# Performance work log

Hardware: AMD Instinct MI355X
Metric: run time of the kernel (lower is better)

Reference implementation:

```python
import jax, jax.numpy as jnp
import numpy as np

B, N, DIM = 1, 1024, 2048
HEADS, KV_HEADS, DH = 16, 2, 128
GQ = HEADS // KV_HEADS
CMP_BLK, CMP_STRIDE = 32, 16
SEL_BLK, N_SEL = 64, 4
WIN = 128
MEM_KV = 1
SCALE = DH ** -0.5
NEG = -1e10


def rmsnorm(x, g):
    return x * jax.lax.rsqrt(jnp.mean(x * x, axis=-1, keepdims=True) + 1e-6) * g


def rope(x):
    # interleaved rotary (rotary-embedding-torch convention), theta=10000
    n, d = x.shape[-2], x.shape[-1]
    inv = 1.0 / (10000.0 ** (jnp.arange(0, d, 2, dtype=jnp.float32) / d))
    ang = jnp.arange(n, dtype=jnp.float32)[:, None] * inv  # (n, d/2)
    cos, sin = jnp.cos(ang), jnp.sin(ang)
    x1, x2 = x[..., 0::2], x[..., 1::2]
    return jnp.stack([x1 * cos - x2 * sin, x1 * sin + x2 * cos], axis=-1).reshape(x.shape)


def _gqa_attend(q, k, v):
    # q: (B, HEADS, N, DH); k, v: (B, KV_HEADS, J, DH). heads split h-major into (kv_h, gq).
    qg = q.reshape(B, KV_HEADS, GQ, N, DH)
    sim = jnp.einsum('bhgnd,bhjd->bhgnj', qg, k) * SCALE
    attn = jax.nn.softmax(sim, axis=-1)
    out = jnp.einsum('bhgnj,bhjd->bhgnd', attn, v)
    return out.reshape(B, HEADS, N, DH), sim


def _fwd(x, g_norm, W_qkv, k_pos, v_pos, mem_kv, Wk1, bk1, Wk2, bk2, Wv1, bv1, Wv2, bv2, Wg, bg, W_out):
    dim_inner = HEADS * DH
    dim_kv = KV_HEADS * DH
    xn = rmsnorm(x, g_norm)
    qkv = xn @ W_qkv
    q, k, v = jnp.split(qkv, [dim_inner, dim_inner + dim_kv], axis=-1)
    q = q.reshape(B, N, HEADS, DH).transpose(0, 2, 1, 3)
    k = k.reshape(B, N, KV_HEADS, DH).transpose(0, 2, 1, 3)
    v = v.reshape(B, N, KV_HEADS, DH).transpose(0, 2, 1, 3)

    # ---- compressed branch (pre-rotary q/k): overlapping windows -> MLP per block ----
    ov = CMP_BLK - CMP_STRIDE
    n_win = N // CMP_STRIDE
    widx = jnp.arange(n_win)[:, None] * CMP_STRIDE + jnp.arange(CMP_BLK)[None, :]
    kp = jnp.pad(k, ((0, 0), (0, 0), (ov, 0), (0, 0)))
    vp = jnp.pad(v, ((0, 0), (0, 0), (ov, 0), (0, 0)))
    kwin = kp[:, :, widx, :] + k_pos[None, :, None]  # (B,KV,n_win,CMP_BLK,DH)
    vwin = vp[:, :, widx, :] + v_pos[None, :, None]

    def mlp(w, W1, b1, W2, b2):
        f = w.reshape(B, KV_HEADS, n_win, CMP_BLK * DH)
        return jax.nn.relu(f @ W1 + b1) @ W2 + b2

    ck = mlp(kwin, Wk1, bk1, Wk2, bk2)
    cv = mlp(vwin, Wv1, bv1, Wv2, bv2)
    ck = jnp.concatenate([jnp.broadcast_to(mem_kv[0][None], (B, KV_HEADS, MEM_KV, DH)), ck], axis=2)
    cv = jnp.concatenate([jnp.broadcast_to(mem_kv[1][None], (B, KV_HEADS, MEM_KV, DH)), cv], axis=2)
    cmp_out, csim = _gqa_attend(q, ck, cv)

    # ---- rotary embeddings for fine + sliding branches ----
    q = rope(q)
    k = rope(k)

    # ---- top-k block selection from compressed similarities ----
    n_fine = N // SEL_BLK
    cpf = SEL_BLK // CMP_STRIDE
    imp = csim[..., MEM_KV:].mean(axis=2)  # (B,KV,N,n_win): mean over grouped queries
    imp = imp.reshape(B, KV_HEADS, N, n_fine, cpf).mean(axis=-1)
    qi = jnp.arange(N) // SEL_BLK
    diag = qi[:, None] == jnp.arange(n_fine)[None, :]
    imp = jnp.where(diag, NEG, imp)  # own block masked out of scoring
    imp = jax.nn.softmax(jnp.pad(imp, ((0, 0), (0, 0), (0, 0), (1, 0)), constant_values=-1000.0), axis=-1)[..., 1:]
    _, sel = jax.lax.top_k(imp, N_SEL)  # (B,KV,N,N_SEL)
    own = jnp.broadcast_to(qi[None, None, :, None], (B, KV_HEADS, N, 1))
    sel = jnp.concatenate([sel, own], axis=-1)  # always attend the query's own block

    # ---- fine (selected-block) attention ----
    kb = k.reshape(B, KV_HEADS, n_fine, SEL_BLK, DH)
    vb = v.reshape(B, KV_HEADS, n_fine, SEL_BLK, DH)
    gather = jax.vmap(jax.vmap(lambda blocks, idx: blocks[idx]))  # over B, KV_HEADS
    t_tot = (N_SEL + 1) * SEL_BLK
    fk = gather(kb, sel).reshape(B, KV_HEADS, N, t_tot, DH)
    fv = gather(vb, sel).reshape(B, KV_HEADS, N, t_tot, DH)
    qg = q.reshape(B, KV_HEADS, GQ, N, DH)
    fsim = jnp.einsum('bhgnd,bhntd->bhgnt', qg, fk) * SCALE
    fattn = jax.nn.softmax(fsim, axis=-1)
    fine_out = jnp.einsum('bhgnt,bhntd->bhgnd', fattn, fv).reshape(B, HEADS, N, DH)

    # ---- sliding window attention (non-causal, exact windowsize) ----
    kf = jnp.repeat(k, GQ, axis=1)
    vf = jnp.repeat(v, GQ, axis=1)
    nb = N // WIN
    qb = q.reshape(B, HEADS, nb, WIN, DH)
    kpad = jnp.pad(kf, ((0, 0), (0, 0), (WIN, WIN), (0, 0))).reshape(B, HEADS, nb + 2, WIN, DH)
    vpad = jnp.pad(vf, ((0, 0), (0, 0), (WIN, WIN), (0, 0))).reshape(B, HEADS, nb + 2, WIN, DH)
    kwin3 = jnp.concatenate([kpad[:, :, i:i + nb] for i in range(3)], axis=3)  # (B,H,nb,3W,DH)
    vwin3 = jnp.concatenate([vpad[:, :, i:i + nb] for i in range(3)], axis=3)
    qoff = jnp.arange(WIN)
    koff = jnp.arange(3 * WIN) - WIN
    rel_ok = jnp.abs(qoff[:, None] - koff[None, :]) <= WIN  # (W, 3W)
    kglob = jnp.arange(nb)[:, None] * WIN + koff[None, :]
    in_range = (kglob >= 0) & (kglob < N)  # (nb, 3W)
    mask = rel_ok[None, :, :] & in_range[:, None, :]  # (nb, W, 3W)
    ssim = jnp.einsum('bhnid,bhnjd->bhnij', qb, kwin3) * SCALE
    ssim = jnp.where(mask, ssim, NEG)
    sattn = jax.nn.softmax(ssim, axis=-1)
    slide_out = jnp.einsum('bhnij,bhnjd->bhnid', sattn, vwin3).reshape(B, HEADS, N, DH)

    # ---- learned sigmoid gate combine: (compressed, fine, sliding) ----
    gates = jax.nn.sigmoid(xn @ Wg + bg).reshape(B, N, HEADS, 3).transpose(0, 2, 1, 3)
    out = cmp_out * gates[..., 0:1] + fine_out * gates[..., 1:2] + slide_out * gates[..., 2:3]
    out = out.transpose(0, 2, 1, 3).reshape(B, N, HEADS * DH)
    return out @ W_out


def setup_inputs():
    key = jax.random.key(0)
    ks = jax.random.split(key, 12)
    s = 0.02
    dim_inner, dim_kv, cdim = HEADS * DH, KV_HEADS * DH, CMP_BLK * DH
    rn = lambda k, shape: jax.random.normal(k, shape, jnp.float32) * s
    return {
        'x': jax.random.normal(ks[0], (B, N, DIM), jnp.float32),
        'g_norm': jnp.ones((DIM,), jnp.float32),
        'W_qkv': rn(ks[1], (DIM, dim_inner + 2 * dim_kv)),
        'k_pos': rn(ks[2], (KV_HEADS, CMP_BLK, DH)),
        'v_pos': rn(ks[3], (KV_HEADS, CMP_BLK, DH)),
        'mem_kv': rn(ks[4], (2, KV_HEADS, MEM_KV, DH)),
        'Wk1': rn(ks[5], (cdim, cdim)), 'bk1': jnp.zeros((cdim,), jnp.float32),
        'Wk2': rn(ks[6], (cdim, DH)), 'bk2': jnp.zeros((DH,), jnp.float32),
        'Wv1': rn(ks[7], (cdim, cdim)), 'bv1': jnp.zeros((cdim,), jnp.float32),
        'Wv2': rn(ks[8], (cdim, DH)), 'bv2': jnp.zeros((DH,), jnp.float32),
        'Wg': rn(ks[9], (DIM, 3 * HEADS)),
        'bg': jnp.tile(jnp.array([-2.0, -2.0, 2.0], jnp.float32), HEADS),
        'W_out': rn(ks[10], (dim_inner, DIM)),
    }


def reference(x, g_norm, W_qkv, k_pos, v_pos, mem_kv, Wk1, bk1, Wk2, bk2, Wv1, bv1, Wv2, bv2, Wg, bg, W_out):
    return _fwd(x, g_norm, W_qkv, k_pos, v_pos, mem_kv, Wk1, bk1, Wk2, bk2, Wv1, bv1, Wv2, bv2, Wg, bg, W_out)
```

## Files before the change

### kernel.cpp

```cpp
#include <hip/hip_runtime.h>
#include <hip/hip_bf16.h>
#include <math.h>

typedef __hip_bfloat16 bf16;
typedef __attribute__((ext_vector_type(8))) short bf16x8;
typedef __attribute__((ext_vector_type(4))) float f32x4;

#define N_TOK 1024
#define DIM 2048
#define NHEADS 16
#define KVH 2
#define DH 128
#define GQ 8
#define NWIN 64
#define CMP_BLK 32
#define NCMP 65
#define NFINE 16
#define SEL_BLK 64
#define T_TOT 320
#define CDIM 4096
#define SCALE 0.08838834764831845f

static __device__ __forceinline__ float b2f(bf16 v){ return __bfloat162float(v); }
static __device__ __forceinline__ float bfbits2f(unsigned int u){
// ... 130 lines not shown
  float* C           = kvsel ? cvb : ckb;
  __shared__ __align__(16) float As[16*68];
  __shared__ __align__(16) float Bs[16*68];
  int tid = threadIdx.x;
  int tx = tid & 15, ty = tid >> 4;
  int m0 = blockIdx.y * 64, n0 = blockIdx.x * 64;
  float c[4][4] = {};
  for (int k0 = kz; k0 < kz + 128; k0 += 16){
    #pragma unroll
    for (int i = 0; i < 4; ++i){
      int idx = tid + i*256;
      int kk = idx & 15, m = idx >> 4;
      float av = Af[(size_t)(m0+m)*CDIM + k0 + kk];
      av = fmaxf(av + afold[k0+kk], 0.f);
      As[kk*68 + m] = av;
    }
    #pragma unroll
    for (int i = 0; i < 4; ++i){
      int idx = tid + i*256;
      int nn = idx & 63, kk = idx >> 6;
      Bs[kk*68 + nn] = B[(size_t)(k0+kk)*DH + n0 + nn];
    }
    __syncthreads();
    #pragma unroll
    for (int kk = 0; kk < 16; ++kk){
      float a[4], b[4];
      *(float4*)a = *(const float4*)&As[kk*68 + ty*4];
      *(float4*)b = *(const float4*)&Bs[kk*68 + tx*4];
      #pragma unroll
      for (int i = 0; i < 4; ++i)
        #pragma unroll
        for (int j = 0; j < 4; ++j)
          c[i][j] += a[i]*b[j];
    }
    __syncthreads();
  }
  #pragma unroll
  for (int i = 0; i < 4; ++i){
    int row = m0 + ty*4 + i;
    #pragma unroll
    for (int j = 0; j < 4; ++j){
      int col = n0 + tx*4 + j;
      atomicAdd(&C[(size_t)row*DH + col], c[i][j]);
    }
  }
}

__global__ __launch_bounds__(256) void gemm_mfma_mlp1_kernel(const unsigned short* __restrict__ fh,
                                                             const unsigned short* __restrict__ fl,
                                                             const float* __restrict__ Wk1,
                                                             const float* __restrict__ Wv1,
                                                             float* __restrict__ hbuf2){
  const int kvsel = blockIdx.z >> 3;
  const int kz = (blockIdx.z & 7) * 512;
  const unsigned short* Ah = fh + (size_t)kvsel*128*CDIM;
  const unsigned short* Al = fl + (size_t)kvsel*128*CDIM;
  const float* B = kvsel ? Wv1 : Wk1;
  float* C = hbuf2 + (size_t)kvsel*128*CDIM;
  const int n0 = blockIdx.x * 64;
  const int m0 = blockIdx.y * 32;
  const int tid = threadIdx.x;
  const int wid = tid >> 6, lane = tid & 63;
  const int l15 = lane & 15, lg = lane >> 4;
  const int colL = wid*16 + l15;
  __shared__ __align__(16) float Bs[2][32][68];

  f32x4 acc[2];
  #pragma unroll
  for (int m = 0; m < 2; ++m) acc[m] = (f32x4){0.f,0.f,0.f,0.f};

  const unsigned short* ahp[2];
  const unsigned short* alp[2];
  #pragma unroll
  for (int m = 0; m < 2; ++m){
    size_t ro = (size_t)(m0 + m*16 + l15)*CDIM + kz + lg*8;
    ahp[m] = Ah + ro;
    alp[m] = Al + ro;
  }
  const int sr = tid >> 3, sc = (tid & 7) * 8;

  float4 rb0, rb1;
  int4 rah[2], ral[2];
  {
    const float* bp = B + (size_t)(kz + sr)*CDIM + n0 + sc;
    rb0 = *(const float4*)(bp);
    rb1 = *(const float4*)(bp + 4);
    #pragma unroll
    for (int m = 0; m < 2; ++m){
      rah[m] = *(const int4*)(ahp[m]);
      ral[m] = *(const int4*)(alp[m]);
    }
  }

  #pragma unroll 1
  for (int s = 0; s < 16; ++s){
    const int buf = s & 1;
    *(float4*)&Bs[buf][sr][sc]     = rb0;
    *(float4*)&Bs[buf][sr][sc + 4] = rb1;
    int4 cah[2], cal[2];
    #pragma unroll
    for (int m = 0; m < 2; ++m){ cah[m] = rah[m]; cal[m] = ral[m]; }
    __syncthreads();
    if (s + 1 < 16){
      const int kr = kz + (s+1)*32;
      const float* bp = B + (size_t)(kr + sr)*CDIM + n0 + sc;
      rb0 = *(const float4*)(bp);
      rb1 = *(const float4*)(bp + 4);
      #pragma unroll
      for (int m = 0; m < 2; ++m){
        rah[m] = *(const int4*)(ahp[m] + (s+1)*32);
        ral[m] = *(const int4*)(alp[m] + (s+1)*32);
      }
    }
    float bv[8];
    #pragma unroll
    for (int j = 0; j < 8; ++j) bv[j] = Bs[buf][lg*8 + j][colL];
    bf16x8 bh, bl;
    #pragma unroll
    for (int j = 0; j < 8; ++j){
      unsigned short h = f2bf(bv[j]);
      bh[j] = (short)h;
      bl[j] = (short)f2bf(bv[j] - bfbits2f(h));
    }
    #pragma unroll
    for (int m = 0; m < 2; ++m){
      union { int4 i; bf16x8 v; } uah, ual;
      uah.i = cah[m]; ual.i = cal[m];
      acc[m] = __builtin_amdgcn_mfma_f32_16x16x32_bf16(uah.v, bh, acc[m], 0, 0, 0);
      acc[m] = __builtin_amdgcn_mfma_f32_16x16x32_bf16(ual.v, bh, acc[m], 0, 0, 0);
      acc[m] = __builtin_amdgcn_mfma_f32_16x16x32_bf16(uah.v, bl, acc[m], 0, 0, 0);
    }
  }
  const int col = n0 + colL;
  #pragma unroll
  for (int m = 0; m < 2; ++m)
    #pragma unroll
    for (int r = 0; r < 4; ++r){
      const int row = m0 + m*16 + lg*4 + r;
      atomicAdd(&C[(size_t)row*CDIM + col], acc[m][r]);
    }
}

__global__ __launch_bounds__(256) void gemm_mfma_qkvT_kernel(const unsigned short* __restrict__ Ah,
                                                             const unsigned short* __restrict__ Al,
                                                             const unsigned short* __restrict__ BhT,
                                                             const unsigned short* __restrict__ BlT,
                                                             float* __restrict__ Cq,
                                                             float* __restrict__ Ckv){
  const int n0 = blockIdx.x * 64;
  const int m0 = blockIdx.y * 32;
  const int tid = threadIdx.x;
  const int wid = tid >> 6, lane = tid & 63;
  const int l15 = lane & 15, lg = lane >> 4;
  const int col = n0 + wid*16 + l15;
  const size_t ASTR = (size_t)N_TOK*32;
  const size_t BSTR = (size_t)2560*32;

  f32x4 acc[2];
  #pragma unroll
  for (int m = 0; m < 2; ++m) acc[m] = (f32x4){0.f,0.f,0.f,0.f};

  const unsigned short* aph[2];
  const unsigned short* apl[2];
  #pragma unroll
  for (int m = 0; m < 2; ++m){
    size_t ro = (size_t)(m0 + m*16 + l15)*32 + lg*8;
    aph[m] = Ah + ro;
    apl[m] = Al + ro;
  }
  const unsigned short* bph = BhT + (size_t)col*32 + lg*8;
  const unsigned short* bpl = BlT + (size_t)col*32 + lg*8;

  int4 rah0[2], ral0[2], rah1[2], ral1[2];
  int4 rbh0, rbl0, rbh1, rbl1;
  #pragma unroll
  for (int m = 0; m < 2; ++m){
    rah0[m] = *(const int4*)(aph[m]);
    ral0[m] = *(const int4*)(apl[m]);
    rah1[m] = *(const int4*)(aph[m] + ASTR);
    ral1[m] = *(const int4*)(apl[m] + ASTR);
  }
  rbh0 = *(const int4*)(bph);
  rbl0 = *(const int4*)(bpl);
  rbh1 = *(const int4*)(bph + BSTR);
  rbl1 = *(const int4*)(bpl + BSTR);

// ... 127 lines not shown
  #pragma unroll
  for (int m = 0; m < 2; ++m)
    #pragma unroll
    for (int r = 0; r < 4; ++r){
      const int row = m0 + m*16 + lg*4 + r;
      C[(size_t)row*DIM + col] = acc[m][r];
    }
}

__global__ __launch_bounds__(256) void rope_kernel(const float* __restrict__ q,
    const float* __restrict__ kv, bf16* __restrict__ qr, bf16* __restrict__ kr){
  int n = blockIdx.x, tid = threadIdx.x;
  const float* qrow = q + (size_t)n*DIM;
  bf16* qrrow = qr + (size_t)n*DIM;
  #pragma unroll
  for (int i = 0; i < 4; ++i){
    int p = tid + i*256;
    int hd = p >> 6, ii = p & 63;
    float inv = powf(10000.f, -(float)ii/64.f);
    float ang = (float)n * inv;
    float cs = cosf(ang), sn = sinf(ang);
    float x1 = qrow[hd*DH + 2*ii], x2 = qrow[hd*DH + 2*ii + 1];
    qrrow[hd*DH + 2*ii]     = __float2bfloat16(x1*cs - x2*sn);
    qrrow[hd*DH + 2*ii + 1] = __float2bfloat16(x1*sn + x2*cs);
  }
  if (tid < 128){
    int h = tid >> 6, ii = tid & 63;
    float inv = powf(10000.f, -(float)ii/64.f);
    float ang = (float)n * inv;
    float cs = cosf(ang), sn = sinf(ang);
    const float* kvrow = kv + (size_t)n*512;
    float x1 = kvrow[h*DH + 2*ii], x2 = kvrow[h*DH + 2*ii + 1];
    bf16* krrow = kr + (size_t)n*256;
    krrow[h*DH + 2*ii]     = __float2bfloat16(x1*cs - x2*sn);
    krrow[h*DH + 2*ii + 1] = __float2bfloat16(x1*sn + x2*cs);
  }
}

__global__ __launch_bounds__(256) void build_f_kernel(const float* __restrict__ kv,
    const float* __restrict__ k_pos, const float* __restrict__ v_pos,
    unsigned short* __restrict__ fh, unsigned short* __restrict__ fl){
  int bw2 = blockIdx.x;
  int kvsel = bw2 >> 7, bw = bw2 & 127;
  int voff = kvsel * 256;
  const float* pos = kvsel ? v_pos : k_pos;
  int h = bw >> 6, w = bw & 63;
  int tid = threadIdx.x;
  for (int idx = tid; idx < CMP_BLK*DH; idx += 256){
    int j = idx >> 7, d = idx & 127;
    int t = w*16 + j - 16;
    float kvv = (t >= 0) ? kv[(size_t)t*512 + voff + h*DH + d] : 0.f;
    float v = kvv + pos[(h*CMP_BLK + j)*DH + d];
    unsigned short hh = f2bf(v);
    size_t o = (size_t)kvsel*128*CDIM + (size_t)bw*CDIM + idx;
    fh[o] = hh;
    fl[o] = f2bf(v - bfbits2f(hh));
  }
}

__global__ __launch_bounds__(256) void assemble_kernel(const float* __restrict__ ckb,
    const float* __restrict__ cvb, const float* __restrict__ mem_kv,
    const float* __restrict__ bk2, const float* __restrict__ bv2,
    float* __restrict__ ck, float* __restrict__ cv){
  int j = blockIdx.x;
  int tid = threadIdx.x;
  int h = tid >> 7, d = tid & 127;
  float kvx, vvx;
  if (j == 0){
    kvx = mem_kv[(0*KVH + h)*DH + d];
    vvx = mem_kv[(1*KVH + h)*DH + d];
  } else {
    kvx = ckb[((size_t)h*NWIN + (j-1))*DH + d] + bk2[d];
    vvx = cvb[((size_t)h*NWIN + (j-1))*DH + d] + bv2[d];
  }
  ck[((size_t)h*NCMP + j)*DH + d] = kvx;
  cv[((size_t)h*NCMP + j)*DH + d] = vvx;
}

__global__ __launch_bounds__(256) void cmp_attn_kernel(const float* __restrict__ q,
    const float* __restrict__ ck, const float* __restrict__ cv,
    bf16* __restrict__ cmp_o, int* __restrict__ sel){
  int bx = blockIdx.x;
  int h = bx >> 10, n = bx & 1023;
  int tid = threadIdx.x;
  __shared__ float cks[NCMP*129];
  __shared__ float qs[GQ*DH];
  __shared__ float sims[GQ*66];
  __shared__ float red[GQ*32];
  __shared__ float impb[NFINE];
  for (int idx = tid; idx < NCMP*DH; idx += 256){
    int j = idx >> 7, d = idx & 127;
    cks[j*129 + d] = ck[((size_t)h*NCMP + j)*DH + d];
  }
  for (int idx = tid; idx < GQ*DH; idx += 256)
    qs[idx] = q[(size_t)n*DIM + h*(GQ*DH) + idx];
  __syncthreads();
  for (int p = tid; p < GQ*NCMP; p += 256){
    int g = p / NCMP, j = p % NCMP;
    float acc = 0.f;
    const float* qp = &qs[g*DH];
    const float* kp = &cks[j*129];
    #pragma unroll 4
    for (int d = 0; d < DH; ++d) acc += qp[d]*kp[d];
    sims[g*66 + j] = acc * SCALE;
  }
  __syncthreads();
  if (tid < NFINE){
    float s = 0.f;
    for (int g = 0; g < GQ; ++g)
      #pragma unroll
      for (int c = 0; c < 4; ++c)
        s += sims[g*66 + 1 + tid*4 + c];
    impb[tid] = s;
  }
  __syncthreads();
  if (tid == 0){
    int own = n >> 6;
    impb[own] = -1e30f;
    int selbuf[5];
    #pragma unroll
    for (int r = 0; r < 4; ++r){
      float best = -1e38f; int bi = 0;
      for (int f = 0; f < NFINE; ++f)
        if (impb[f] > best){ best = impb[f]; bi = f; }
      selbuf[r] = bi; impb[bi] = -1e38f;
    }
    selbuf[4] = own;
    for (int r = 0; r < 5; ++r) sel[(size_t)(h*N_TOK + n)*8 + r] = selbuf[r];
  }
  int g = tid >> 5, lane = tid & 31;
  float m = -1e38f;
  for (int j = lane; j < NCMP; j += 32) m = fmaxf(m, sims[g*66 + j]);
  red[g*32 + lane] = m; __syncthreads();
  for (int st = 16; st > 0; st >>= 1){ if (lane < st) red[g*32+lane] = fmaxf(red[g*32+lane], red[g*32+lane+st]); __syncthreads(); }
  float gm = red[g*32]; __syncthreads();
  float ps = 0.f;
  for (int j = lane; j < NCMP; j += 32){ float e = expf(sims[g*66+j] - gm); sims[g*66+j] = e; ps += e; }
  red[g*32+lane] = ps; __syncthreads();
  for (int st = 16; st > 0; st >>= 1){ if (lane < st) red[g*32+lane] += red[g*32+lane+st]; __syncthreads(); }
  float inv = 1.f / red[g*32]; __syncthreads();
  for (int j = lane; j < NCMP; j += 32) sims[g*66+j] *= inv;
  __syncthreads();
  for (int p = tid; p < GQ*DH; p += 256){
    int gg = p >> 7, d = p & 127;
    float acc = 0.f;
    const float* cvp = cv + (size_t)h*NCMP*DH + d;
    for (int j = 0; j < NCMP; ++j) acc += sims[gg*66 + j] * cvp[j*DH];
    cmp_o[(size_t)n*DIM + (h*GQ + gg)*DH + d] = __float2bfloat16(acc);
  }
}

__global__ __launch_bounds__(256) void fine_attn_kernel(const bf16* __restrict__ qr,
    const bf16* __restrict__ kr, const float* __restrict__ kv,
    const int* __restrict__ sel, bf16* __restrict__ fine_o){
  int bx = blockIdx.x;
  int h = bx >> 10, n = bx & 1023;
  int tid = threadIdx.x;
  __shared__ __align__(16) float kvbuf[8448];
  __shared__ __align__(16) float qs[GQ*DH];
  __shared__ float sims[GQ*322];
  __shared__ float red[GQ*32];
  const int qi = tid >> 5, tx = tid & 31;

  int sel5[5];
  #pragma unroll
  for (int r = 0; r < 5; ++r){
    int b = sel[(size_t)(h*N_TOK + n)*8 + r];
    sel5[r] = (b < 0) ? 0 : (b > 15 ? 15 : b);
  }
  for (int idx = tid; idx < GQ*DH; idx += 256)
    qs[idx] = b2f(qr[(size_t)n*DIM + h*(GQ*DH) + idx]);

  for (int tile = 0; tile < 5; ++tile){
    int blk = sel5[tile];
    __syncthreads();
    for (int c = tid; c < 1024; c += 256){
      int t = c & 63, d0 = (c >> 6) << 3;
      int4 w = *(const int4*)(kr + (size_t)(blk*SEL_BLK + t)*256 + h*DH + d0);
      float* dst = &kvbuf[(size_t)d0*66 + t];
      unsigned int wv[4] = {(unsigned)w.x,(unsigned)w.y,(unsigned)w.z,(unsigned)w.w};
      #pragma unroll
      for (int m = 0; m < 4; ++m){
        dst[(2*m  )*66] = bfbits2f(wv[m] & 0xffffu);
        dst[(2*m+1)*66] = bfbits2f(wv[m] >> 16);
      }
    }
    __syncthreads();
    float acc0 = 0.f, acc1 = 0.f;
    const float* qp = &qs[qi*DH];
    const float* kp = &kvbuf[2*tx];
    #pragma unroll
    for (int d = 0; d < DH; d += 4){
      float4 a = *(const float4*)(qp + d);
      float2 b0 = *(const float2*)(kp + (size_t)(d  )*66);
      float2 b1 = *(const float2*)(kp + (size_t)(d+1)*66);
      float2 b2 = *(const float2*)(kp + (size_t)(d+2)*66);
      float2 b3 = *(const float2*)(kp + (size_t)(d+3)*66);
      acc0 += a.x*b0.x; acc1 += a.x*b0.y;
      acc0 += a.y*b1.x; acc1 += a.y*b1.y;
      acc0 += a.z*b2.x; acc1 += a.z*b2.y;
      acc0 += a.w*b3.x; acc1 += a.w*b3.y;
    }
    *(float2*)&sims[(size_t)qi*322 + tile*SEL_BLK + 2*tx] = make_float2(acc0*SCALE, acc1*SCALE);
  }
  __syncthreads();

  {
    int g = qi, lane = tx;
    float m = -1e38f;
    for (int t = lane; t < T_TOT; t += 32) m = fmaxf(m, sims[g*322 + t]);
    red[g*32+lane] = m; __syncthreads();
    for (int st = 16; st > 0; st >>= 1){ if (lane < st) red[g*32+lane] = fmaxf(red[g*32+lane], red[g*32+lane+st]); __syncthreads(); }
    float gm = red[g*32]; __syncthreads();
    float ps = 0.f;
    for (int t = lane; t < T_TOT; t += 32){ float e = expf(sims[g*322+t] - gm); sims[g*322+t] = e; ps += e; }
    red[g*32+lane] = ps; __syncthreads();
    for (int st = 16; st > 0; st >>= 1){ if (lane < st) red[g*32+lane] += red[g*32+lane+st]; __syncthreads(); }
    float inv = 1.f / red[g*32]; __syncthreads();
    for (int t = lane; t < T_TOT; t += 32) sims[g*322+t] *= inv;
  }

  float av[4] = {0.f,0.f,0.f,0.f};
  for (int tile = 0; tile < 5; ++tile){
    int blk = sel5[tile];
    __syncthreads();
    for (int c = tid; c < 2048; c += 256){
      int t = c >> 5, d0 = (c & 31) << 2;
      float4 v = *(const float4*)(kv + (size_t)(blk*SEL_BLK + t)*512 + 256 + h*DH + d0);
      *(float4*)&kvbuf[(size_t)t*132 + d0] = v;
    }
    __syncthreads();
    const float* sp = &sims[(size_t)qi*322 + tile*SEL_BLK];
    const float* vp = &kvbuf[tx << 2];
    #pragma unroll 8
    for (int t = 0; t < SEL_BLK; ++t){
      float p = sp[t];
      float4 v = *(const float4*)(vp + (size_t)t*132);
      av[0] += p*v.x; av[1] += p*v.y; av[2] += p*v.z; av[3] += p*v.w;
    }
  }
  {
    bf16 o[4];
    o[0] = __float2bfloat16(av[0]);
    o[1] = __float2bfloat16(av[1]);
    o[2] = __float2bfloat16(av[2]);
    o[3] = __float2bfloat16(av[3]);
    *(ushort4*)(fine_o + (size_t)n*DIM + (h*GQ + qi)*DH + (tx << 2)) = *(const ushort4*)o;
  }
}

__global__ __launch_bounds__(256) void slide_attn_kernel(const bf16* __restrict__ qr,
    const bf16* __restrict__ kr, const float* __restrict__ kv,
    bf16* __restrict__ slide_o){
  int hq = blockIdx.y;
  int qt = blockIdx.x;
  int h = hq >> 3;
  int n0 = qt * 32;
  int tid = threadIdx.x;
  __shared__ float qT[128*36];
  __shared__ float kvb[128*68];
  __shared__ float stT[64*36];

  const int ty  = tid >> 5;
  const int tx  = tid & 31;
  const int qi0 = ty << 2;

  for (int c = tid; c < 512; c += 256){
    int qi = c & 31, d0 = (c >> 5) << 3;
    int4 w = *(const int4*)(qr + (size_t)(n0+qi)*DIM + hq*DH + d0);
    float* dst = &qT[(size_t)d0*36 + qi];
    unsigned int wv[4] = {(unsigned)w.x,(unsigned)w.y,(unsigned)w.z,(unsigned)w.w};
    #pragma unroll
    for (int m = 0; m < 4; ++m){
      dst[(2*m  )*36] = bfbits2f(wv[m] & 0xffffu);
      dst[(2*m+1)*36] = bfbits2f(wv[m] >> 16);
    }
  }

  float acc[4][4] = {};
  float mrow[4] = {-1e30f,-1e30f,-1e30f,-1e30f};
  float lrow[4] = {0.f,0.f,0.f,0.f};
  float arow[4];
  const int kstart = n0 - 128;

  for (int tile = 0; tile < 5; ++tile){
    const int kbase = kstart + tile*64;
    __syncthreads();
    for (int c = tid; c < 1024; c += 256){
      int t = c & 63, d0 = (c >> 6) << 3;
      int kg = kbase + t;
      int kgc = min(max(kg, 0), N_TOK-1);
      int4 w = *(const int4*)(kr + (size_t)kgc*256 + h*DH + d0);
      float* dst = &kvb[(size_t)d0*68 + t];
      unsigned int wv[4] = {(unsigned)w.x,(unsigned)w.y,(unsigned)w.z,(unsigned)w.w};
      #pragma unroll
      for (int m = 0; m < 4; ++m){
        dst[(2*m  )*68] = bfbits2f(wv[m] & 0xffffu);
        dst[(2*m+1)*68] = bfbits2f(wv[m] >> 16);
      }
// ... 70 lines not shown
  for (int i = 0; i < 4; ++i){
    int row = n0 + qi0 + i;
    float inv = 1.f / lrow[i];
    bf16 o[4];
    o[0] = __float2bfloat16(acc[i][0]*inv);
    o[1] = __float2bfloat16(acc[i][1]*inv);
    o[2] = __float2bfloat16(acc[i][2]*inv);
    o[3] = __float2bfloat16(acc[i][3]*inv);
    *(ushort4*)(slide_o + (size_t)row*DIM + hq*DH + (tx << 2)) = *(const ushort4*)o;
  }
}

__global__ __launch_bounds__(256) void combine_kernel(const bf16* __restrict__ cmp_o,
    const bf16* __restrict__ fine_o, const bf16* __restrict__ slide_o,
    const float* __restrict__ graw, const float* __restrict__ bg,
    unsigned short* __restrict__ ocombT){
  int n = blockIdx.x, tid = threadIdx.x;
  #pragma unroll
  for (int i = 0; i < 8; ++i){
    int c = tid + i*256;
    int hq = c >> 7;
    float g0 = 1.f/(1.f + expf(-(graw[(size_t)n*48 + hq*3 + 0] + bg[hq*3 + 0])));
    float g1 = 1.f/(1.f + expf(-(graw[(size_t)n*48 + hq*3 + 1] + bg[hq*3 + 1])));
    float g2 = 1.f/(1.f + expf(-(graw[(size_t)n*48 + hq*3 + 2] + bg[hq*3 + 2])));
    size_t idx = (size_t)n*DIM + c;
    float v = b2f(cmp_o[idx])*g0 + b2f(fine_o[idx])*g1 + b2f(slide_o[idx])*g2;
    int sl = c >> 5, kk = c & 31;
    ocombT[(size_t)sl*(N_TOK*32) + (size_t)n*32 + kk] = f2bf(v);
  }
}

extern "C" void kernel_launch(void* const* d_in, const int* in_sizes, int n_in,
                              void* d_out, int out_size, void* d_ws, size_t ws_size,
                              hipStream_t stream)
{
  const float* x      = (const float*)d_in[0];
  const float* g_norm = (const float*)d_in[1];
  const float* W_qkv  = (const float*)d_in[2];
  const float* k_pos  = (const float*)d_in[3];
  const float* v_pos  = (const float*)d_in[4];
  const float* mem_kv = (const float*)d_in[5];
  const float* Wk1    = (const float*)d_in[6];
  const float* bk1    = (const float*)d_in[7];
  const float* Wk2    = (const float*)d_in[8];
  const float* bk2    = (const float*)d_in[9];
  const float* Wv1    = (const float*)d_in[10];
  const float* bv1    = (const float*)d_in[11];
  const float* Wv2    = (const float*)d_in[12];
  const float* bv2    = (const float*)d_in[13];
  const float* Wg     = (const float*)d_in[14];
  const float* bg     = (const float*)d_in[15];
  const float* W_out  = (const float*)d_in[16];
  float* out = (float*)d_out;
  (void)ws_size; (void)in_sizes; (void)n_in; (void)out_size;

  char* base = (char*)d_ws;
  float* q     = (float*)(base + 0);
  float* xn    = (float*)(base + 8388608);
  bf16*  qr    = (bf16*) (base + 8388608);
  bf16*  kr    = (bf16*) (base + 12582912);
  unsigned short* ocombT = (unsigned short*)(base + 8388608);
  float* kv    = (float*)(base + 16777216);
  float* hbuf2 = (float*)(base + 18874368);
  bf16*  cmp_o = (bf16*) (base + 18874368);
  float* ckb   = (float*)(base + 23068672);
  float* cvb   = (float*)(base + 23134208);
  float* ck    = (float*)(base + 23199744);
  float* cv    = (float*)(base + 23266304);
  float* gates = (float*)(base + 23332864);
  int*   sel   = (int*)  (base + 23529472);
  bf16*  fine_o  = (bf16*)(base + 0);
  bf16*  slide_o = (bf16*)(base + 4194304);
  unsigned short* xnh  = (unsigned short*)(base + 25165824);
  unsigned short* xnl  = (unsigned short*)(base + 29360128);
  unsigned short* WqhT = (unsigned short*)(base + 33554432);
  unsigned short* WqlT = (unsigned short*)(base + 44040192);
  unsigned short* WohT = WqhT;
  unsigned short* WolT = WqlT;
  unsigned short* fh   = (unsigned short*)(base + 41943040);
  unsigned short* fl   = (unsigned short*)(base + 52428800);

  hipMemsetAsync(gates, 0, (size_t)N_TOK*48*4,   stream);
  hipMemsetAsync(ckb,   0, (size_t)KVH*NWIN*DH*4, stream);
  hipMemsetAsync(cvb,   0, (size_t)KVH*NWIN*DH*4, stream);
  hipMemsetAsync(hbuf2, 0, (size_t)2*128*CDIM*4,  stream);

  transpose_split_kernel<<<dim3(40, 32), 256, 0, stream>>>(W_qkv, 2560, 2560, WqhT, WqlT);
  rmsnorm_kernel<<<N_TOK, 256, 0, stream>>>(x, g_norm, xn, xnh, xnl);
  gemm_splitk_kernel<<<dim3(1, 16, 16), 256, 0, stream>>>(xn, 0, nullptr, Wg, 48, gates, N_TOK, 48, DIM, 128);
  gemm_mfma_qkvT_kernel<<<dim3(40, 32), 256, 0, stream>>>(xnh, xnl, WqhT, WqlT, q, kv);
  transpose_split_kernel<<<dim3(32, 32), 256, 0, stream>>>(W_out, 2048, 2048, WohT, WolT);
  rope_kernel<<<N_TOK, 256, 0, stream>>>(q, kv, qr, kr);
  build_f_kernel<<<256, 256, 0, stream>>>(kv, k_pos, v_pos, fh, fl);
  gemm_mfma_mlp1_kernel<<<dim3(64, 4, 16), 256, 0, stream>>>(fh, fl, Wk1, Wv1, hbuf2);
  gemm_mlp2_fused_kernel<<<dim3(2, 2, 64), 256, 0, stream>>>(hbuf2, bk1, bv1, Wk2, Wv2, ckb, cvb);
  assemble_kernel<<<NCMP, 256, 0, stream>>>(ckb, cvb, mem_kv, bk2, bv2, ck, cv);
  cmp_attn_kernel<<<KVH*N_TOK, 256, 0, stream>>>(q, ck, cv, cmp_o, sel);
  fine_attn_kernel<<<KVH*N_TOK, 256, 0, stream>>>(qr, kr, kv, sel, fine_o);
  slide_attn_kernel<<<dim3(32, 16), 256, 0, stream>>>(qr, kr, kv, slide_o);
  combine_kernel<<<N_TOK, 256, 0, stream>>>(cmp_o, fine_o, slide_o, gates, bg, ocombT);
  gemm_mfma_outT_kernel<<<dim3(32, 32), 256, 0, stream>>>(ocombT, WohT, WolT, out);
}
```

Before: 787.2 us.

## Pre-split MLP1 weights into bf16 hi/lo slabs and use slab-major layout

Rearranges the compressed-window feature buffer into a K-slab-major layout (32-wide slabs). Adds a path that converts Wk1/Wv1 each call into transposed bf16 hi/lo slab buffers, so the MLP1 GEMM can load MFMA operands straight from global memory without LDS staging or per-iteration float-to-bf16 splitting. The old kernel is kept as a fallback when the workspace is too small. The trade is two extra 4096x4096 transpose-split passes per call (about 128MB of extra writes) against a cheaper inner loop with fewer split-K blocks.

```diff
diff --git a/kernel.cpp b/kernel.cpp
--- a/kernel.cpp
+++ b/kernel.cpp
@@ -206,11 +206,12 @@
                                                              const float* __restrict__ Wv1,
                                                              float* __restrict__ hbuf2){
   const int kvsel = blockIdx.z >> 3;
-  const int kz = (blockIdx.z & 7) * 512;
-  const unsigned short* Ah = fh + (size_t)kvsel*128*CDIM;
-  const unsigned short* Al = fl + (size_t)kvsel*128*CDIM;
+  const int slab0 = (blockIdx.z & 7) * 16;
+  const int kz = slab0 * 32;
+  const unsigned short* Ah = fh + (size_t)kvsel*524288 + (size_t)slab0*4096;
+  const unsigned short* Al = fl + (size_t)kvsel*524288 + (size_t)slab0*4096;
   const float* B = kvsel ? Wv1 : Wk1;
-  float* C = hbuf2 + (size_t)kvsel*128*CDIM;
+  float* C = hbuf2 + (size_t)kvsel*524288;
   const int n0 = blockIdx.x * 64;
   const int m0 = blockIdx.y * 32;
   const int tid = threadIdx.x;
@@ -227,7 +228,7 @@
   const unsigned short* alp[2];
   #pragma unroll
   for (int m = 0; m < 2; ++m){
-    size_t ro = (size_t)(m0 + m*16 + l15)*CDIM + kz + lg*8;
+    size_t ro = (size_t)(m0 + m*16 + l15)*32 + lg*8;
     ahp[m] = Ah + ro;
     alp[m] = Al + ro;
   }
@@ -262,8 +263,8 @@
       rb1 = *(const float4*)(bp + 4);
       #pragma unroll
       for (int m = 0; m < 2; ++m){
-        rah[m] = *(const int4*)(ahp[m] + (s+1)*32);
-        ral[m] = *(const int4*)(alp[m] + (s+1)*32);
+        rah[m] = *(const int4*)(ahp[m] + (size_t)(s+1)*4096);
+        ral[m] = *(const int4*)(alp[m] + (size_t)(s+1)*4096);
       }
     }
     float bv[8];
@@ -286,6 +287,110 @@
     }
   }
   const int col = n0 + colL;
+  #pragma unroll
+  for (int m = 0; m < 2; ++m)
+    #pragma unroll
+    for (int r = 0; r < 4; ++r){
+      const int row = m0 + m*16 + lg*4 + r;
+      atomicAdd(&C[(size_t)row*CDIM + col], acc[m][r]);
+    }
+}
+
+__global__ __launch_bounds__(256) void gemm_mfma_mlp1T_kernel(const unsigned short* __restrict__ fh,
+    const unsigned short* __restrict__ fl,
+    const unsigned short* __restrict__ Wk1h, const unsigned short* __restrict__ Wk1l,
+    const unsigned short* __restrict__ Wv1h, const unsigned short* __restrict__ Wv1l,
+    float* __restrict__ hbuf2){
+  const int kvsel = blockIdx.z >> 2;
+  const int slab0 = (blockIdx.z & 3) * 32;
+  const unsigned short* Ahb = fh + (size_t)kvsel*524288 + (size_t)slab0*4096;
+  const unsigned short* Alb = fl + (size_t)kvsel*524288 + (size_t)slab0*4096;
+  const unsigned short* Bhb = (kvsel ? Wv1h : Wk1h) + (size_t)slab0*131072;
+  const unsigned short* Blb = (kvsel ? Wv1l : Wk1l) + (size_t)slab0*131072;
+  float* C = hbuf2 + (size_t)kvsel*524288;
+  const int n0 = blockIdx.x * 64;
+  const int m0 = blockIdx.y * 32;
+  const int tid = threadIdx.x;
+  const int wid = tid >> 6, lane = tid & 63;
+  const int l15 = lane & 15, lg = lane >> 4;
+  const int col = n0 + wid*16 + l15;
+  const size_t ASTR = 4096;
+  const size_t BSTR = 131072;
+
+  f32x4 acc[2];
+  #pragma unroll
+  for (int m = 0; m < 2; ++m) acc[m] = (f32x4){0.f,0.f,0.f,0.f};
+
+  const unsigned short* aph[2];
+  const unsigned short* apl[2];
+  #pragma unroll
+  for (int m = 0; m < 2; ++m){
+    size_t ro = (size_t)(m0 + m*16 + l15)*32 + lg*8;
+    aph[m] = Ahb + ro;
+    apl[m] = Alb + ro;
+  }
+  const unsigned short* bph = Bhb + (size_t)col*32 + lg*8;
+  const unsigned short* bpl = Blb + (size_t)col*32 + lg*8;
+
+  int4 rah0[2], ral0[2], rah1[2], ral1[2];
+  int4 rbh0, rbl0, rbh1, rbl1;
+  #pragma unroll
+  for (int m = 0; m < 2; ++m){
+    rah0[m] = *(const int4*)(aph[m]);
+    ral0[m] = *(const int4*)(apl[m]);
+    rah1[m] = *(const int4*)(aph[m] + ASTR);
+    ral1[m] = *(const int4*)(apl[m] + ASTR);
+  }
+  rbh0 = *(const int4*)(bph);
+  rbl0 = *(const int4*)(bpl);
+  rbh1 = *(const int4*)(bph + BSTR);
+  rbl1 = *(const int4*)(bpl + BSTR);
+
+  #pragma unroll 1
+  for (int s = 0; s < 32; s += 2){
+    {
+      union { int4 i; bf16x8 v; } ubh, ubl;
+      ubh.i = rbh0; ubl.i = rbl0;
+      #pragma unroll
+      for (int m = 0; m < 2; ++m){
+        union { int4 i; bf16x8 v; } uah, ual;
+        uah.i = rah0[m]; ual.i = ral0[m];
+        acc[m] = __builtin_amdgcn_mfma_f32_16x16x32_bf16(uah.v, ubh.v, acc[m], 0, 0, 0);
+        acc[m] = __builtin_amdgcn_mfma_f32_16x16x32_bf16(ual.v, ubh.v, acc[m], 0, 0, 0);
+        acc[m] = __builtin_amdgcn_mfma_f32_16x16x32_bf16(uah.v, ubl.v, acc[m], 0, 0, 0);
+      }
+    }
+    if (s + 2 < 32){
+      #pragma unroll
+      for (int m = 0; m < 2; ++m){
+        rah0[m] = *(const int4*)(aph[m] + (size_t)(s+2)*ASTR);
+        ral0[m] = *(const int4*)(apl[m] + (size_t)(s+2)*ASTR);
+      }
+      rbh0 = *(const int4*)(bph + (size_t)(s+2)*BSTR);
+      rbl0 = *(const int4*)(bpl + (size_t)(s+2)*BSTR);
+    }
+    {
+      union { int4 i; bf16x8 v; } ubh, ubl;
+      ubh.i = rbh1; ubl.i = rbl1;
+      #pragma unroll
+      for (int m = 0; m < 2; ++m){
+        union { int4 i; bf16x8 v; } uah, ual;
+        uah.i = rah1[m]; ual.i = ral1[m];
+        acc[m] = __builtin_amdgcn_mfma_f32_16x16x32_bf16(uah.v, ubh.v, acc[m], 0, 0, 0);
+        acc[m] = __builtin_amdgcn_mfma_f32_16x16x32_bf16(ual.v, ubh.v, acc[m], 0, 0, 0);
+        acc[m] = __builtin_amdgcn_mfma_f32_16x16x32_bf16(uah.v, ubl.v, acc[m], 0, 0, 0);
+      }
+    }
+    if (s + 3 < 32){
+      #pragma unroll
+      for (int m = 0; m < 2; ++m){
+        rah1[m] = *(const int4*)(aph[m] + (size_t)(s+3)*ASTR);
+        ral1[m] = *(const int4*)(apl[m] + (size_t)(s+3)*ASTR);
+      }
+      rbh1 = *(const int4*)(bph + (size_t)(s+3)*BSTR);
+      rbl1 = *(const int4*)(bpl + (size_t)(s+3)*BSTR);
+    }
+  }
   #pragma unroll
   for (int m = 0; m < 2; ++m)
     #pragma unroll
@@ -519,7 +624,8 @@
     float kvv = (t >= 0) ? kv[(size_t)t*512 + voff + h*DH + d] : 0.f;
     float v = kvv + pos[(h*CMP_BLK + j)*DH + d];
     unsigned short hh = f2bf(v);
-    size_t o = (size_t)kvsel*128*CDIM + (size_t)bw*CDIM + idx;
+    int sl = idx >> 5, kk = idx & 31;
+    size_t o = (size_t)kvsel*524288 + (size_t)sl*4096 + (size_t)bw*32 + kk;
     fh[o] = hh;
     fl[o] = f2bf(v - bfbits2f(hh));
   }
@@ -888,7 +994,7 @@
   const float* bg     = (const float*)d_in[15];
   const float* W_out  = (const float*)d_in[16];
   float* out = (float*)d_out;
-  (void)ws_size; (void)in_sizes; (void)n_in; (void)out_size;
+  (void)in_sizes; (void)n_in; (void)out_size;
 
   char* base = (char*)d_ws;
   float* q     = (float*)(base + 0);
@@ -915,6 +1021,12 @@
   unsigned short* WolT = WqlT;
   unsigned short* fh   = (unsigned short*)(base + 41943040);
   unsigned short* fl   = (unsigned short*)(base + 52428800);
+  const size_t W1BASE = 56623104ull;
+  unsigned short* Wk1h = (unsigned short*)(base + W1BASE);
+  unsigned short* Wk1l = (unsigned short*)(base + W1BASE +  33554432ull);
+  unsigned short* Wv1h = (unsigned short*)(base + W1BASE +  67108864ull);
+  unsigned short* Wv1l = (unsigned short*)(base + W1BASE + 100663296ull);
+  const bool presplit = ws_size >= (W1BASE + 134217728ull);
 
   hipMemsetAsync(gates, 0, (size_t)N_TOK*48*4,   stream);
   hipMemsetAsync(ckb,   0, (size_t)KVH*NWIN*DH*4, stream);
@@ -928,7 +1040,13 @@
   transpose_split_kernel<<<dim3(32, 32), 256, 0, stream>>>(W_out, 2048, 2048, WohT, WolT);
   rope_kernel<<<N_TOK, 256, 0, stream>>>(q, kv, qr, kr);
   build_f_kernel<<<256, 256, 0, stream>>>(kv, k_pos, v_pos, fh, fl);
-  gemm_mfma_mlp1_kernel<<<dim3(64, 4, 16), 256, 0, stream>>>(fh, fl, Wk1, Wv1, hbuf2);
+  if (presplit){
+    transpose_split_kernel<<<dim3(64, 64), 256, 0, stream>>>(Wk1, CDIM, CDIM, Wk1h, Wk1l);
+    transpose_split_kernel<<<dim3(64, 64), 256, 0, stream>>>(Wv1, CDIM, CDIM, Wv1h, Wv1l);
+    gemm_mfma_mlp1T_kernel<<<dim3(64, 4, 8), 256, 0, stream>>>(fh, fl, Wk1h, Wk1l, Wv1h, Wv1l, hbuf2);
+  } else {
+    gemm_mfma_mlp1_kernel<<<dim3(64, 4, 16), 256, 0, stream>>>(fh, fl, Wk1, Wv1, hbuf2);
+  }
   gemm_mlp2_fused_kernel<<<dim3(2, 2, 64), 256, 0, stream>>>(hbuf2, bk1, bv1, Wk2, Wv2, ckb, cvb);
   assemble_kernel<<<NCMP, 256, 0, stream>>>(ckb, cvb, mem_kv, bk2, bv2, ck, cv);
   cmp_attn_kernel<<<KVH*N_TOK, 256, 0, stream>>>(q, ck, cv, cmp_o, sel);
```

Result: slower. 806.0 us (+2.4%).

## Slab-major layout for MLP1 A operand and register-prefetch fine attention tiles

Applied to the files above, without the earlier changes.

Reorders the bf16 hi/lo window features built by build_f_kernel into 32-column k-slabs so each MLP1 GEMM block reads contiguous 32-element rows per step instead of strided CDIM rows. Separately, the fine selected-block attention kernel now prefetches the next K and V tiles into registers while computing on the current tile, overlapping global loads with compute. The prefetch adds register pressure (12 int4/float4 per thread), which may lower occupancy.

```diff
diff --git a/kernel.cpp b/kernel.cpp
--- a/kernel.cpp
+++ b/kernel.cpp
@@ -206,11 +206,12 @@
                                                              const float* __restrict__ Wv1,
                                                              float* __restrict__ hbuf2){
   const int kvsel = blockIdx.z >> 3;
-  const int kz = (blockIdx.z & 7) * 512;
-  const unsigned short* Ah = fh + (size_t)kvsel*128*CDIM;
-  const unsigned short* Al = fl + (size_t)kvsel*128*CDIM;
+  const int slab0 = (blockIdx.z & 7) * 16;
+  const int kz = slab0 * 32;
+  const unsigned short* Ah = fh + (size_t)kvsel*524288 + (size_t)slab0*4096;
+  const unsigned short* Al = fl + (size_t)kvsel*524288 + (size_t)slab0*4096;
   const float* B = kvsel ? Wv1 : Wk1;
-  float* C = hbuf2 + (size_t)kvsel*128*CDIM;
+  float* C = hbuf2 + (size_t)kvsel*524288;
   const int n0 = blockIdx.x * 64;
   const int m0 = blockIdx.y * 32;
   const int tid = threadIdx.x;
@@ -227,7 +228,7 @@
   const unsigned short* alp[2];
   #pragma unroll
   for (int m = 0; m < 2; ++m){
-    size_t ro = (size_t)(m0 + m*16 + l15)*CDIM + kz + lg*8;
+    size_t ro = (size_t)(m0 + m*16 + l15)*32 + lg*8;
     ahp[m] = Ah + ro;
     alp[m] = Al + ro;
   }
@@ -262,8 +263,8 @@
       rb1 = *(const float4*)(bp + 4);
       #pragma unroll
       for (int m = 0; m < 2; ++m){
-        rah[m] = *(const int4*)(ahp[m] + (s+1)*32);
-        ral[m] = *(const int4*)(alp[m] + (s+1)*32);
+        rah[m] = *(const int4*)(ahp[m] + (size_t)(s+1)*4096);
+        ral[m] = *(const int4*)(alp[m] + (size_t)(s+1)*4096);
       }
     }
     float bv[8];
@@ -519,7 +520,8 @@
     float kvv = (t >= 0) ? kv[(size_t)t*512 + voff + h*DH + d] : 0.f;
     float v = kvv + pos[(h*CMP_BLK + j)*DH + d];
     unsigned short hh = f2bf(v);
-    size_t o = (size_t)kvsel*128*CDIM + (size_t)bw*CDIM + idx;
+    int sl = idx >> 5, kk = idx & 31;
+    size_t o = (size_t)kvsel*524288 + (size_t)sl*4096 + (size_t)bw*32 + kk;
     fh[o] = hh;
     fl[o] = f2bf(v - bfbits2f(hh));
   }
@@ -638,14 +640,24 @@
   for (int idx = tid; idx < GQ*DH; idx += 256)
     qs[idx] = b2f(qr[(size_t)n*DIM + h*(GQ*DH) + idx]);
 
+  int4 kreg[4];
+  {
+    int blk = sel5[0];
+    #pragma unroll
+    for (int i = 0; i < 4; ++i){
+      int c = tid + i*256;
+      int t = c & 63, d0 = (c >> 6) << 3;
+      kreg[i] = *(const int4*)(kr + (size_t)(blk*SEL_BLK + t)*256 + h*DH + d0);
+    }
+  }
   for (int tile = 0; tile < 5; ++tile){
-    int blk = sel5[tile];
-    __syncthreads();
-    for (int c = tid; c < 1024; c += 256){
+    __syncthreads();
+    #pragma unroll
+    for (int i = 0; i < 4; ++i){
+      int c = tid + i*256;
       int t = c & 63, d0 = (c >> 6) << 3;
-      int4 w = *(const int4*)(kr + (size_t)(blk*SEL_BLK + t)*256 + h*DH + d0);
+      unsigned int wv[4] = {(unsigned)kreg[i].x,(unsigned)kreg[i].y,(unsigned)kreg[i].z,(unsigned)kreg[i].w};
       float* dst = &kvbuf[(size_t)d0*66 + t];
-      unsigned int wv[4] = {(unsigned)w.x,(unsigned)w.y,(unsigned)w.z,(unsigned)w.w};
       #pragma unroll
       for (int m = 0; m < 4; ++m){
         dst[(2*m  )*66] = bfbits2f(wv[m] & 0xffffu);
@@ -653,6 +665,15 @@
       }
     }
     __syncthreads();
+    if (tile + 1 < 5){
+      int blk = sel5[tile+1];
+      #pragma unroll
+      for (int i = 0; i < 4; ++i){
+        int c = tid + i*256;
+        int t = c & 63, d0 = (c >> 6) << 3;
+        kreg[i] = *(const int4*)(kr + (size_t)(blk*SEL_BLK + t)*256 + h*DH + d0);
+      }
+    }
     float acc0 = 0.f, acc1 = 0.f;
     const float* qp = &qs[qi*DH];
     const float* kp = &kvbuf[2*tx];
@@ -669,6 +690,17 @@
       acc0 += a.w*b3.x; acc1 += a.w*b3.y;
     }
     *(float2*)&sims[(size_t)qi*322 + tile*SEL_BLK + 2*tx] = make_float2(acc0*SCALE, acc1*SCALE);
+  }
+
+  float4 vreg[8];
+  {
+    int blk = sel5[0];
+    #pragma unroll
+    for (int i = 0; i < 8; ++i){
+      int c = tid + i*256;
+      int t = c >> 5, d0 = (c & 31) << 2;
+      vreg[i] = *(const float4*)(kv + (size_t)(blk*SEL_BLK + t)*512 + 256 + h*DH + d0);
+    }
   }
   __syncthreads();
 
@@ -689,14 +721,23 @@
 
   float av[4] = {0.f,0.f,0.f,0.f};
   for (int tile = 0; tile < 5; ++tile){
-    int blk = sel5[tile];
-    __syncthreads();
-    for (int c = tid; c < 2048; c += 256){
+    __syncthreads();
+    #pragma unroll
+    for (int i = 0; i < 8; ++i){
+      int c = tid + i*256;
       int t = c >> 5, d0 = (c & 31) << 2;
-      float4 v = *(const float4*)(kv + (size_t)(blk*SEL_BLK + t)*512 + 256 + h*DH + d0);
-      *(float4*)&kvbuf[(size_t)t*132 + d0] = v;
-    }
-    __syncthreads();
+      *(float4*)&kvbuf[(size_t)t*132 + d0] = vreg[i];
+    }
+    __syncthreads();
+    if (tile + 1 < 5){
+      int blk = sel5[tile+1];
+      #pragma unroll
+      for (int i = 0; i < 8; ++i){
+        int c = tid + i*256;
+        int t = c >> 5, d0 = (c & 31) << 2;
+        vreg[i] = *(const float4*)(kv + (size_t)(blk*SEL_BLK + t)*512 + 256 + h*DH + d0);
+      }
+    }
     const float* sp = &sims[(size_t)qi*322 + tile*SEL_BLK];
     const float* vp = &kvbuf[tx << 2];
     #pragma unroll 8
```

New measurement: 785.2 us. Within noise of the previous version (-0.2%).

## Prefetch next selected K/V tile in fine attention; slab-major layout for MLP1 A operand

Applied to the files above, without the earlier changes.

The fine attention kernel now loads the next selected block's K (and later V) into registers while computing on the current tile in shared memory, software-pipelining global loads against compute. Separately, the compressed-MLP input buffers are rewritten in a slab-major layout (32-wide K slabs) so each GEMM step reads a contiguous chunk instead of strided rows. This raises register pressure in the fine kernel and changes producer and consumer layouts together.

```diff
diff --git a/kernel.cpp b/kernel.cpp
--- a/kernel.cpp
+++ b/kernel.cpp
@@ -206,11 +206,12 @@
                                                              const float* __restrict__ Wv1,
                                                              float* __restrict__ hbuf2){
   const int kvsel = blockIdx.z >> 3;
-  const int kz = (blockIdx.z & 7) * 512;
-  const unsigned short* Ah = fh + (size_t)kvsel*128*CDIM;
-  const unsigned short* Al = fl + (size_t)kvsel*128*CDIM;
+  const int slab0 = (blockIdx.z & 7) * 16;
+  const int kz = slab0 * 32;
+  const unsigned short* Ah = fh + (size_t)kvsel*524288 + (size_t)slab0*4096;
+  const unsigned short* Al = fl + (size_t)kvsel*524288 + (size_t)slab0*4096;
   const float* B = kvsel ? Wv1 : Wk1;
-  float* C = hbuf2 + (size_t)kvsel*128*CDIM;
+  float* C = hbuf2 + (size_t)kvsel*524288;
   const int n0 = blockIdx.x * 64;
   const int m0 = blockIdx.y * 32;
   const int tid = threadIdx.x;
@@ -227,7 +228,7 @@
   const unsigned short* alp[2];
   #pragma unroll
   for (int m = 0; m < 2; ++m){
-    size_t ro = (size_t)(m0 + m*16 + l15)*CDIM + kz + lg*8;
+    size_t ro = (size_t)(m0 + m*16 + l15)*32 + lg*8;
     ahp[m] = Ah + ro;
     alp[m] = Al + ro;
   }
@@ -262,8 +263,8 @@
       rb1 = *(const float4*)(bp + 4);
       #pragma unroll
       for (int m = 0; m < 2; ++m){
-        rah[m] = *(const int4*)(ahp[m] + (s+1)*32);
-        ral[m] = *(const int4*)(alp[m] + (s+1)*32);
+        rah[m] = *(const int4*)(ahp[m] + (size_t)(s+1)*4096);
+        ral[m] = *(const int4*)(alp[m] + (size_t)(s+1)*4096);
       }
     }
     float bv[8];
@@ -519,7 +520,8 @@
     float kvv = (t >= 0) ? kv[(size_t)t*512 + voff + h*DH + d] : 0.f;
     float v = kvv + pos[(h*CMP_BLK + j)*DH + d];
     unsigned short hh = f2bf(v);
-    size_t o = (size_t)kvsel*128*CDIM + (size_t)bw*CDIM + idx;
+    int sl = idx >> 5, kk = idx & 31;
+    size_t o = (size_t)kvsel*524288 + (size_t)sl*4096 + (size_t)bw*32 + kk;
     fh[o] = hh;
     fl[o] = f2bf(v - bfbits2f(hh));
   }
@@ -617,6 +619,73 @@
   }
 }
 
+#define FA_LOADK(blk) do{ \
+    const bf16* p_ = kr + (size_t)((blk)*SEL_BLK + tK)*256 + h*DH; \
+    k0 = *(const int4*)(p_ + dK);      \
+    k1 = *(const int4*)(p_ + dK + 32); \
+    k2 = *(const int4*)(p_ + dK + 64); \
+    k3 = *(const int4*)(p_ + dK + 96); \
+  }while(0)
+#define FA_STOREK1(reg, db) do{ \
+    unsigned w0_=(unsigned)(reg).x, w1_=(unsigned)(reg).y, w2_=(unsigned)(reg).z, w3_=(unsigned)(reg).w; \
+    float* d_ = &kvbuf[(size_t)(db)*66 + tK]; \
+    d_[0]   = bfbits2f(w0_ & 0xffffu); d_[66]  = bfbits2f(w0_ >> 16); \
+    d_[132] = bfbits2f(w1_ & 0xffffu); d_[198] = bfbits2f(w1_ >> 16); \
+    d_[264] = bfbits2f(w2_ & 0xffffu); d_[330] = bfbits2f(w2_ >> 16); \
+    d_[396] = bfbits2f(w3_ & 0xffffu); d_[462] = bfbits2f(w3_ >> 16); \
+  }while(0)
+#define FA_STOREK do{ FA_STOREK1(k0,(dK)); FA_STOREK1(k1,(dK+32)); FA_STOREK1(k2,(dK+64)); FA_STOREK1(k3,(dK+96)); }while(0)
+#define FA_QK(tile) do{ \
+    float acc0_ = 0.f, acc1_ = 0.f; \
+    const float* qp_ = &qs[qi*DH]; \
+    const float* kp_ = &kvbuf[2*tx]; \
+    _Pragma("unroll") \
+    for (int d_ = 0; d_ < DH; d_ += 4){ \
+      float4 a_ = *(const float4*)(qp_ + d_); \
+      float2 b0_ = *(const float2*)(kp_ + (size_t)(d_  )*66); \
+      float2 b1_ = *(const float2*)(kp_ + (size_t)(d_+1)*66); \
+      float2 b2_ = *(const float2*)(kp_ + (size_t)(d_+2)*66); \
+      float2 b3_ = *(const float2*)(kp_ + (size_t)(d_+3)*66); \
+      acc0_ += a_.x*b0_.x; acc1_ += a_.x*b0_.y; \
+      acc0_ += a_.y*b1_.x; acc1_ += a_.y*b1_.y; \
+      acc0_ += a_.z*b2_.x; acc1_ += a_.z*b2_.y; \
+      acc0_ += a_.w*b3_.x; acc1_ += a_.w*b3_.y; \
+    } \
+    *(float2*)&sims[(size_t)qi*322 + (tile)*SEL_BLK + 2*tx] = make_float2(acc0_*SCALE, acc1_*SCALE); \
+  }while(0)
+#define FA_LOADV(blk) do{ \
+    const float* p_ = kv + (size_t)((blk)*SEL_BLK + tV)*512 + 256 + h*DH; \
+    v0 = *(const float4*)(p_ + dV);         \
+    v1 = *(const float4*)(p_ + 4096 + dV);  \
+    v2 = *(const float4*)(p_ + 8192 + dV);  \
+    v3 = *(const float4*)(p_ + 12288 + dV); \
+    v4 = *(const float4*)(p_ + 16384 + dV); \
+    v5 = *(const float4*)(p_ + 20480 + dV); \
+    v6 = *(const float4*)(p_ + 24576 + dV); \
+    v7 = *(const float4*)(p_ + 28672 + dV); \
+  }while(0)
+#define FA_STOREV do{ \
+    float* d_ = &kvbuf[(size_t)tV*132 + dV]; \
+    *(float4*)(d_)        = v0; \
+    *(float4*)(d_ + 1056) = v1; \
+    *(float4*)(d_ + 2112) = v2; \
+    *(float4*)(d_ + 3168) = v3; \
+    *(float4*)(d_ + 4224) = v4; \
+    *(float4*)(d_ + 5280) = v5; \
+    *(float4*)(d_ + 6336) = v6; \
+    *(float4*)(d_ + 7392) = v7; \
+  }while(0)
+#define FA_PV(tile) do{ \
+    const float* sp_ = &sims[(size_t)qi*322 + (tile)*SEL_BLK]; \
+    const float* vp_ = &kvbuf[tx << 2]; \
+    _Pragma("unroll 8") \
+    for (int t_ = 0; t_ < SEL_BLK; ++t_){ \
+      float p_ = sp_[t_]; \
+      float4 vv_ = *(const float4*)(vp_ + (size_t)t_*132); \
+      av0 += p_*vv_.x; av1 += p_*vv_.y; av2 += p_*vv_.z; av3 += p_*vv_.w; \
+    } \
+  }while(0)
+
 __global__ __launch_bounds__(256) void fine_attn_kernel(const bf16* __restrict__ qr,
     const bf16* __restrict__ kr, const float* __restrict__ kv,
     const int* __restrict__ sel, bf16* __restrict__ fine_o){
@@ -629,47 +698,33 @@
   __shared__ float red[GQ*32];
   const int qi = tid >> 5, tx = tid & 31;
 
-  int sel5[5];
-  #pragma unroll
-  for (int r = 0; r < 5; ++r){
-    int b = sel[(size_t)(h*N_TOK + n)*8 + r];
-    sel5[r] = (b < 0) ? 0 : (b > 15 ? 15 : b);
+  int s0_, s1_, s2_, s3_, s4_;
+  {
+    const int* sp = sel + (size_t)(h*N_TOK + n)*8;
+    int b0 = sp[0], b1 = sp[1], b2 = sp[2], b3 = sp[3], b4 = sp[4];
+    s0_ = (b0 < 0) ? 0 : (b0 > 15 ? 15 : b0);
+    s1_ = (b1 < 0) ? 0 : (b1 > 15 ? 15 : b1);
+    s2_ = (b2 < 0) ? 0 : (b2 > 15 ? 15 : b2);
+    s3_ = (b3 < 0) ? 0 : (b3 > 15 ? 15 : b3);
+    s4_ = (b4 < 0) ? 0 : (b4 > 15 ? 15 : b4);
   }
   for (int idx = tid; idx < GQ*DH; idx += 256)
     qs[idx] = b2f(qr[(size_t)n*DIM + h*(GQ*DH) + idx]);
 
-  for (int tile = 0; tile < 5; ++tile){
-    int blk = sel5[tile];
-    __syncthreads();
-    for (int c = tid; c < 1024; c += 256){
-      int t = c & 63, d0 = (c >> 6) << 3;
-      int4 w = *(const int4*)(kr + (size_t)(blk*SEL_BLK + t)*256 + h*DH + d0);
-      float* dst = &kvbuf[(size_t)d0*66 + t];
-      unsigned int wv[4] = {(unsigned)w.x,(unsigned)w.y,(unsigned)w.z,(unsigned)w.w};
-      #pragma unroll
-      for (int m = 0; m < 4; ++m){
-        dst[(2*m  )*66] = bfbits2f(wv[m] & 0xffffu);
-        dst[(2*m+1)*66] = bfbits2f(wv[m] >> 16);
-      }
-    }
-    __syncthreads();
-    float acc0 = 0.f, acc1 = 0.f;
-    const float* qp = &qs[qi*DH];
-    const float* kp = &kvbuf[2*tx];
-    #pragma unroll
-    for (int d = 0; d < DH; d += 4){
-      float4 a = *(const float4*)(qp + d);
-      float2 b0 = *(const float2*)(kp + (size_t)(d  )*66);
-      float2 b1 = *(const float2*)(kp + (size_t)(d+1)*66);
-      float2 b2 = *(const float2*)(kp + (size_t)(d+2)*66);
-      float2 b3 = *(const float2*)(kp + (size_t)(d+3)*66);
-      acc0 += a.x*b0.x; acc1 += a.x*b0.y;
-      acc0 += a.y*b1.x; acc1 += a.y*b1.y;
-      acc0 += a.z*b2.x; acc1 += a.z*b2.y;
-      acc0 += a.w*b3.x; acc1 += a.w*b3.y;
-    }
-    *(float2*)&sims[(size_t)qi*322 + tile*SEL_BLK + 2*tx] = make_float2(acc0*SCALE, acc1*SCALE);
-  }
+  const int tK = tid & 63;
+  const int dK = (tid >> 6) << 3;
+  int4 k0, k1, k2, k3;
+  FA_LOADK(s0_);
+  __syncthreads(); FA_STOREK; __syncthreads(); FA_LOADK(s1_); FA_QK(0);
+  __syncthreads(); FA_STOREK; __syncthreads(); FA_LOADK(s2_); FA_QK(1);
+  __syncthreads(); FA_STOREK; __syncthreads(); FA_LOADK(s3_); FA_QK(2);
+  __syncthreads(); FA_STOREK; __syncthreads(); FA_LOADK(s4_); FA_QK(3);
+  __syncthreads(); FA_STOREK; __syncthreads();                FA_QK(4);
+
+  const int tV = tid >> 5;
+  const int dV = (tid & 31) << 2;
+  float4 v0, v1, v2, v3, v4, v5, v6, v7;
+  FA_LOADV(s0_);
   __syncthreads();
 
   {
@@ -687,31 +742,18 @@
     for (int t = lane; t < T_TOT; t += 32) sims[g*322+t] *= inv;
   }
 
-  float av[4] = {0.f,0.f,0.f,0.f};
-  for (int tile = 0; tile < 5; ++tile){
-    int blk = sel5[tile];
-    __syncthreads();
-    for (int c = tid; c < 2048; c += 256){
-      int t = c >> 5, d0 = (c & 31) << 2;
-      float4 v = *(const float4*)(kv + (size_t)(blk*SEL_BLK + t)*512 + 256 + h*DH + d0);
-      *(float4*)&kvbuf[(size_t)t*132 + d0] = v;
-    }
-    __syncthreads();
-    const float* sp = &sims[(size_t)qi*322 + tile*SEL_BLK];
-    const float* vp = &kvbuf[tx << 2];
-    #pragma unroll 8
-    for (int t = 0; t < SEL_BLK; ++t){
-      float p = sp[t];
-      float4 v = *(const float4*)(vp + (size_t)t*132);
-      av[0] += p*v.x; av[1] += p*v.y; av[2] += p*v.z; av[3] += p*v.w;
-    }
-  }
+  float av0 = 0.f, av1 = 0.f, av2 = 0.f, av3 = 0.f;
+  __syncthreads(); FA_STOREV; __syncthreads(); FA_LOADV(s1_); FA_PV(0);
+  __syncthreads(); FA_STOREV; __syncthreads(); FA_LOADV(s2_); FA_PV(1);
+  __syncthreads(); FA_STOREV; __syncthreads(); FA_LOADV(s3_); FA_PV(2);
+  __syncthreads(); FA_STOREV; __syncthreads(); FA_LOADV(s4_); FA_PV(3);
+  __syncthreads(); FA_STOREV; __syncthreads();                FA_PV(4);
   {
     bf16 o[4];
-    o[0] = __float2bfloat16(av[0]);
-    o[1] = __float2bfloat16(av[1]);
-    o[2] = __float2bfloat16(av[2]);
-    o[3] = __float2bfloat16(av[3]);
+    o[0] = __float2bfloat16(av0);
+    o[1] = __float2bfloat16(av1);
+    o[2] = __float2bfloat16(av2);
+    o[3] = __float2bfloat16(av3);
     *(ushort4*)(fine_o + (size_t)n*DIM + (h*GQ + qi)*DH + (tx << 2)) = *(const ushort4*)o;
   }
 }
```

New measurement: 736.2 us. 6.5% less time.
